# Optimization experiments

Measured on AMD Instinct MI355X. Metric: run time of the kernel, lower is better.

## Reference

```python
import jax, jax.numpy as jnp
import numpy as np

B, S, V, E, H, NL, DFF = 16, 16, 64, 64, 8, 4, 2048
L = S * V
DH = E // H
NUM_GRIDS = 100
POI_DIM = 8
OV_DIM = 8


def setup_inputs() -> dict:
    key = jax.random.key(0)
    ks = jax.random.split(key, 32)
    sc = 0.05
    inp = {}
    inp['features'] = jax.random.normal(ks[0], (B, S, V, 3), jnp.float32)
    inp['overlap_tag'] = jax.random.randint(ks[1], (B, S, V), 0, 3)
    inp['poi_id'] = jax.random.randint(ks[2], (B, S, V), 0, NUM_GRIDS + 1)
    # embedders
    inp['W_raw'] = jax.random.normal(ks[3], (3, E), jnp.float32) * sc
    inp['b_raw'] = jnp.zeros((E,), jnp.float32)
    inp['pos_tab'] = jax.random.normal(ks[4], (S, E), jnp.float32) * sc
    inp['type_tab'] = jax.random.normal(ks[5], (V, E), jnp.float32) * sc
    inp['poi_tab'] = jax.random.normal(ks[6], (NUM_GRIDS + 1, POI_DIM), jnp.float32) * sc
    inp['overlap_tab'] = jax.random.normal(ks[7], (3, OV_DIM), jnp.float32) * sc
    inp['W_comb'] = jax.random.normal(ks[8], (E + OV_DIM + POI_DIM, E), jnp.float32) * sc
    inp['b_comb'] = jnp.zeros((E,), jnp.float32)
    # transformer layers (stacked over NL)
    inp['Wqkv'] = jax.random.normal(ks[9], (NL, E, 3 * E), jnp.float32) * sc
    inp['bqkv'] = jnp.zeros((NL, 3 * E), jnp.float32)
    inp['Wo'] = jax.random.normal(ks[10], (NL, E, E), jnp.float32) * sc
    inp['bo'] = jnp.zeros((NL, E), jnp.float32)
    inp['ln1_s'] = jnp.ones((NL, E), jnp.float32)
    inp['ln1_b'] = jnp.zeros((NL, E), jnp.float32)
    inp['W1'] = jax.random.normal(ks[11], (NL, E, DFF), jnp.float32) * sc
    inp['b1'] = jnp.zeros((NL, DFF), jnp.float32)
    inp['W2'] = jax.random.normal(ks[12], (NL, DFF, E), jnp.float32) * sc
    inp['b2'] = jnp.zeros((NL, E), jnp.float32)
    inp['ln2_s'] = jnp.ones((NL, E), jnp.float32)
    inp['ln2_b'] = jnp.zeros((NL, E), jnp.float32)
    inp['W_head'] = jax.random.normal(ks[13], (E, 3), jnp.float32) * sc
    inp['b_head'] = jnp.zeros((3,), jnp.float32)
    return inp


def _layer_norm(x, s, b):
    m = x.mean(-1, keepdims=True)
    v = ((x - m) ** 2).mean(-1, keepdims=True)
    return (x - m) / jnp.sqrt(v + 1e-5) * s + b


def _forward(features, overlap_tag, poi_id, W_raw, b_raw, pos_tab, type_tab,
             poi_tab, overlap_tab, W_comb, b_comb, Wqkv, bqkv, Wo, bo,
             ln1_s, ln1_b, W1, b1, W2, b2, ln2_s, ln2_b, W_head, b_head):
    # padding_idx=0 rows are zero (as in nn.Embedding(padding_idx=0))
    poi_tab = poi_tab.at[0].set(0.0)
    overlap_tab = overlap_tab.at[0].set(0.0)

    zero_mask = (features.sum(-1) == 0).reshape(B, L)  # [B, L]
    ov_idx = jnp.maximum(overlap_tag, 0)
    poi_idx = jnp.maximum(poi_id, 0)

    feat_e = features @ W_raw + b_raw                    # [B,S,V,E]
    concat = jnp.concatenate([feat_e, overlap_tab[ov_idx], poi_tab[poi_idx]], axis=-1)
    x = (concat @ W_comb + b_comb).reshape(B, L, E)      # [B,L,E]

    t_idx = jnp.repeat(jnp.arange(S), V)                 # [L]
    v_idx = jnp.tile(jnp.arange(V), S)                   # [L]
    struct_mask = (t_idx[:, None] != t_idx[None, :]) & (v_idx[:, None] != v_idx[None, :])
    full_mask = struct_mask[None] | zero_mask[:, None, :] | zero_mask[:, :, None]  # [B,L,L]
    bias = jnp.where(full_mask, -jnp.inf, 0.0)[:, None, :, :]  # [B,1,L,L]

    x = x + pos_tab[t_idx][None] + type_tab[v_idx][None]

    scale = 1.0 / jnp.sqrt(jnp.asarray(DH, x.dtype))
    for l in range(NL):
        qkv = x @ Wqkv[l] + bqkv[l]                      # [B,L,3E]
        q, k, v = jnp.split(qkv, 3, axis=-1)
        q = q.reshape(B, L, H, DH)
        k = k.reshape(B, L, H, DH)
        v = v.reshape(B, L, H, DH)
        scores = jnp.einsum('bqhd,bkhd->bhqk', q, k) * scale + bias
        attn = jax.nn.softmax(scores, axis=-1)
        o = jnp.einsum('bhqk,bkhd->bqhd', attn, v).reshape(B, L, E)
        x = _layer_norm(x + o @ Wo[l] + bo[l], ln1_s[l], ln1_b[l])
        ff = jax.nn.relu(x @ W1[l] + b1[l]) @ W2[l] + b2[l]
        x = _layer_norm(x + ff, ln2_s[l], ln2_b[l])

    last = x.reshape(B, S, V, E)[:, -1]                  # [B,V,E]
    return last @ W_head + b_head                        # [B,V,3]


def reference(features, overlap_tag, poi_id, W_raw, b_raw, pos_tab, type_tab,
              poi_tab, overlap_tab, W_comb, b_comb, Wqkv, bqkv, Wo, bo,
              ln1_s, ln1_b, W1, b1, W2, b2, ln2_s, ln2_b, W_head, b_head):
    return _forward(features, overlap_tag, poi_id, W_raw, b_raw, pos_tab, type_tab,
                    poi_tab, overlap_tab, W_comb, b_comb, Wqkv, bqkv, Wo, bo,
                    ln1_s, ln1_b, W1, b1, W2, b2, ln2_s, ln2_b, W_head, b_head)
```

## Files before the change

kernel.cpp:

```cpp
#include <hip/hip_runtime.h>
#include <math.h>

#define BB 16
#define SS 16
#define VVV 64
#define EE 64
#define HHH 8
#define NLAYER 4
#define DFF_ 2048
#define LL 1024
#define BL 16384
#define PERL 131072

typedef __attribute__((ext_vector_type(8))) _Float16 half8;
typedef __attribute__((ext_vector_type(4))) _Float16 half4v;
typedef __attribute__((ext_vector_type(2))) _Float16 half2v;
typedef __attribute__((ext_vector_type(4))) float f32x4;

#if defined(__has_builtin)
#if __has_builtin(__builtin_amdgcn_fdot2)
#define HAVE_FDOT2 1
#endif
#endif

#define SW64(m, k)  (((m) << 6) + ((((k) >> 3) ^ ((m) & 7)) << 3) + ((k) & 7))


__global__ __launch_bounds__(256) void k_prep(
    const float* __restrict__ W1, const float* __restrict__ W2,
    const float* __restrict__ Wqkv, const float* __restrict__ Wo,
    const float* __restrict__ Wcomb,
    _Float16* __restrict__ w1f, _Float16* __restrict__ w2f,
    _Float16* __restrict__ wqkvf, _Float16* __restrict__ wof,
    _Float16* __restrict__ wcombt)
{
  __shared__ float t[64 * 65];
  int bx = blockIdx.x;
  int cc = threadIdx.x & 63, rr = threadIdx.x >> 6;

  if (bx >= 272) {
    int r0 = (bx - 272) * 64;
#pragma unroll
    for (int i = 0; i < 16; i++) {
      int r = i * 4 + rr;
      if (r0 + r < 80) t[r * 65 + cc] = Wcomb[(size_t)(r0 + r) * 64 + cc];
    }
    __syncthreads();
#pragma unroll
    for (int i = 0; i < 16; i++) {
      int c = i * 4 + rr;
      if (r0 + c < 80) wcombt[(size_t)cc * 80 + r0 + c] = (_Float16)t[c * 65 + cc];
    }
    return;
  }

  const float* src; _Float16* dst; int astr;
  if (bx < 128) {
    int l = bx >> 5, g = bx & 31;
    src = W1 + (size_t)l * PERL + g * 64; astr = 2048;
    dst = w1f + (size_t)(l * 32 + g) * 4096;
  } else if (bx < 256) {
    int j = bx - 128; int l = j >> 5, g = j & 31;
    src = W2 + (size_t)l * PERL + (size_t)g * 64 * 64; astr = 64;
    dst = w2f + (size_t)(l * 32 + g) * 4096;
  } else if (bx < 268) {
    int j = bx - 256; int l = j / 3, g = j % 3;
    src = Wqkv + (size_t)l * 64 * 192 + g * 64; astr = 192;
    dst = wqkvf + (size_t)(l * 3 + g) * 4096;
  } else {
    int l = bx - 268;
    src = Wo + (size_t)l * 4096; astr = 64;
    dst = wof + (size_t)l * 4096;
  }
#pragma unroll
  for (int i = 0; i < 16; i++) {
    int a = i * 4 + rr;
    t[cc * 65 + a] = src[(size_t)a * astr + cc];
  }
  __syncthreads();
#pragma unroll
  for (int it = 0; it < 2; it++) {
    int c = threadIdx.x + it * 256;
    int frag = c >> 6, lane = c & 63;
    int m = (frag >> 1) * 16 + (lane & 15);
    int k0 = (frag & 1) * 32 + (lane >> 4) * 8;
    const float* tr = &t[m * 65 + k0];
    half8 h;
#pragma unroll
    for (int j = 0; j < 8; j++) h[j] = (_Float16)tr[j];
    *(half8*)&dst[(size_t)c * 8] = h;
  }
}

__device__ __forceinline__ void qkv_nb(
    const half8 (&af)[2][2], const _Float16* __restrict__ wqkvf,
    const float* __restrict__ bqkv, _Float16* __restrict__ qbuf,
    _Float16* __restrict__ kbuf, _Float16* __restrict__ vbuf,
    int bx, int nb, int wm, int wn, int lane)
{
  int quad = lane >> 4, l15 = lane & 15;
  const _Float16* bt = wqkvf + (size_t)nb * 4096;
  half8 bf[2][2];
#pragma unroll
  for (int nt = 0; nt < 2; nt++)
#pragma unroll
    for (int ks = 0; ks < 2; ks++)
      bf[nt][ks] = *(const half8*)&bt[(size_t)(((wn * 2 + nt) * 2 + ks) * 512) +
                                      lane * 8];
  f32x4 acc[2][2];
#pragma unroll
  for (int mt = 0; mt < 2; mt++)
#pragma unroll
    for (int nt = 0; nt < 2; nt++) {
      float bv = bqkv[nb * 64 + wn * 32 + nt * 16 + l15];
      acc[mt][nt] = (f32x4){bv, bv, bv, bv};
    }
#pragma unroll
  for (int ks = 0; ks < 2; ks++)
#pragma unroll
    for (int mt = 0; mt < 2; mt++)
#pragma unroll
      for (int nt = 0; nt < 2; nt++)
        acc[mt][nt] = __builtin_amdgcn_mfma_f32_16x16x32_f16(
            af[mt][ks], bf[nt][ks], acc[mt][nt], 0, 0, 0);
  _Float16* dst = (nb == 0) ? qbuf : ((nb == 1) ? kbuf : vbuf);
#pragma unroll
  for (int mt = 0; mt < 2; mt++)
#pragma unroll
    for (int nt = 0; nt < 2; nt++) {
      int col = wn * 32 + nt * 16 + l15;
      int h = col >> 3, d = col & 7;
#pragma unroll
      for (int r = 0; r < 4; r++) {
        int row = bx * 64 + wm * 32 + mt * 16 + quad * 4 + r;
        int b = row >> 10, rb = row & 1023;
        dst[((size_t)(b * 8 + h) * 1024 + rb) * 8 + d] = (_Float16)acc[mt][nt][r];
      }
    }
}

__device__ __forceinline__ void ffn_load2(
    const _Float16* __restrict__ w1f, const _Float16* __restrict__ w2f, int g,
    half8 (&a1)[2][2], half8 (&b2w)[2][2], int wn, int lane)
{
  const _Float16* w1t_ = w1f + (size_t)g * 4096;
  const _Float16* w2t_ = w2f + (size_t)g * 4096;
#pragma unroll
  for (int ht = 0; ht < 2; ht++)
#pragma unroll
    for (int ks = 0; ks < 2; ks++)
      a1[ht][ks] = *(const half8*)&w1t_[(size_t)(((wn * 2 + ht) * 2 + ks) * 512) +
                                        lane * 8];
#pragma unroll
  for (int nt = 0; nt < 2; nt++)
#pragma unroll
    for (int ks = 0; ks < 2; ks++)
      b2w[nt][ks] = *(const half8*)&w2t_[(size_t)(((wn * 2 + nt) * 2 + ks) * 512) +
                                         lane * 8];
}

__device__ __forceinline__ void ffn_step2(
    const half8 (&a1)[2][2], const half8 (&b2w)[2][2], const half8 (&xb)[2][2],
    _Float16* hsbuf, const float* __restrict__ b1, int g, f32x4 (&acc)[2][2],
    int wn, int lane)
{
  int quad = lane >> 4, l15 = lane & 15;
  f32x4 hacc[2][2];
#pragma unroll
  for (int ht = 0; ht < 2; ht++)
#pragma unroll
    for (int mt = 0; mt < 2; mt++) hacc[ht][mt] = (f32x4){0.f, 0.f, 0.f, 0.f};
#pragma unroll
  for (int ks = 0; ks < 2; ks++)
#pragma unroll
    for (int ht = 0; ht < 2; ht++)
#pragma unroll
      for (int mt = 0; mt < 2; mt++)
        hacc[ht][mt] = __builtin_amdgcn_mfma_f32_16x16x32_f16(
            a1[ht][ks], xb[mt][ks], hacc[ht][mt], 0, 0, 0);
#pragma unroll
  for (int ht = 0; ht < 2; ht++) {
    float4 bb = *(const float4*)&b1[g * 64 + wn * 32 + ht * 16 + quad * 4];
#pragma unroll
    for (int mt = 0; mt < 2; mt++) {
      f32x4 hv = hacc[ht][mt];
      half4v hp = (half4v){
          (_Float16)fmaxf(hv[0] + bb.x, 0.f), (_Float16)fmaxf(hv[1] + bb.y, 0.f),
          (_Float16)fmaxf(hv[2] + bb.z, 0.f), (_Float16)fmaxf(hv[3] + bb.w, 0.f)};
      *(half4v*)&hsbuf[SW64(mt * 16 + l15, wn * 32 + ht * 16 + quad * 4)] = hp;
    }
  }
  __syncthreads();
#pragma unroll
  for (int ks = 0; ks < 2; ks++)
#pragma unroll
    for (int mt = 0; mt < 2; mt++) {
      half8 a2 = *(const half8*)&hsbuf[SW64(mt * 16 + l15, ks * 32 + quad * 8)];
#pragma unroll
      for (int nt = 0; nt < 2; nt++)
        acc[mt][nt] = __builtin_amdgcn_mfma_f32_16x16x32_f16(a2, b2w[nt][ks],
                                                             acc[mt][nt], 0, 0, 0);
    }
}

__global__ __launch_bounds__(256) void k_embqkv(
    const float* __restrict__ features, const int* __restrict__ ovtag,
    const int* __restrict__ poiid, const float* __restrict__ W_raw,
    const float* __restrict__ b_raw, const float* __restrict__ ov_tab,
    const float* __restrict__ poi_tab, const _Float16* __restrict__ wcombt,
    const float* __restrict__ b_comb, const float* __restrict__ pos_tab,
    const float* __restrict__ type_tab, float* __restrict__ x1,
    float* __restrict__ zm, const _Float16* __restrict__ wqkvf,
    const float* __restrict__ bqkv, _Float16* __restrict__ qbuf,
    _Float16* __restrict__ kbuf, _Float16* __restrict__ vbuf)
{
  constexpr int KP = 104;
  __shared__ _Float16 As[64 * KP];
  __shared__ _Float16 Bs[64 * KP];
  __shared__ _Float16 xs[4096];
  int tid = threadIdx.x;
  int bx = blockIdx.x;
  int m0 = bx * 64;
  int wave = tid >> 6, lane = tid & 63, quad = lane >> 4, l15 = lane & 15;
  int wm = wave >> 1, wn = wave & 1;
  for (int p = tid; p < 1536; p += 256) {
    int r = p / 24, s = p - r * 24; int c = s * 4;
    int row = m0 + r;
    float f0 = features[row * 3 + 0];
    float f1 = features[row * 3 + 1];
    float f2 = features[row * 3 + 2];
    if (s == 0) zm[row] = ((f0 + f1 + f2) == 0.f) ? 1.f : 0.f;
    half4v h;
#pragma unroll
    for (int j = 0; j < 4; j++) {
      int cc = c + j; float v;
      if (cc < 64) {
        v = b_raw[cc] + f0 * W_raw[cc] + f1 * W_raw[64 + cc] + f2 * W_raw[128 + cc];
      } else if (cc < 72) {
        int tt = ovtag[row]; v = (tt <= 0) ? 0.f : ov_tab[tt * 8 + cc - 64];
      } else if (cc < 80) {
        int tt = poiid[row]; v = (tt <= 0) ? 0.f : poi_tab[tt * 8 + cc - 72];
      } else v = 0.f;
      h[j] = (_Float16)v;
    }
    *(half4v*)&As[r * KP + c] = h;
  }
  for (int p = tid; p < 1536; p += 256) {
    int r = p / 24, s = p - r * 24; int c = s * 4;
    half4v h = (half4v){0, 0, 0, 0};
    if (c < 80) h = *(const half4v*)&wcombt[r * 80 + c];
    *(half4v*)&Bs[r * KP + c] = h;
  }
  __syncthreads();
  f32x4 acc[2][2];
#pragma unroll
  for (int mt = 0; mt < 2; mt++)
#pragma unroll
    for (int nt = 0; nt < 2; nt++) {
      float bv = b_comb[wn * 32 + nt * 16 + l15];
      acc[mt][nt] = (f32x4){bv, bv, bv, bv};
    }
#pragma unroll
  for (int ks = 0; ks < 3; ks++) {
    half8 af[2], bf[2];
#pragma unroll
    for (int mt = 0; mt < 2; mt++)
      af[mt] = *(const half8*)&As[(wm * 32 + mt * 16 + l15) * KP + ks * 32 + quad * 8];
#pragma unroll
    for (int nt = 0; nt < 2; nt++)
      bf[nt] = *(const half8*)&Bs[(wn * 32 + nt * 16 + l15) * KP + ks * 32 + quad * 8];
#pragma unroll
    for (int mt = 0; mt < 2; mt++)
#pragma unroll
      for (int nt = 0; nt < 2; nt++)
        acc[mt][nt] = __builtin_amdgcn_mfma_f32_16x16x32_f16(af[mt], bf[nt],
                                                             acc[mt][nt], 0, 0, 0);
  }
#pragma unroll
  for (int mt = 0; mt < 2; mt++)
#pragma unroll
    for (int nt = 0; nt < 2; nt++)
#pragma unroll
      for (int r = 0; r < 4; r++) {
        int lrow = wm * 32 + mt * 16 + quad * 4 + r;
        int row = m0 + lrow;
        int col = wn * 32 + nt * 16 + l15;
        int l = row & (LL - 1);
        float v = acc[mt][nt][r] +
            pos_tab[(l >> 6) * 64 + col] + type_tab[(l & 63) * 64 + col];
        x1[(size_t)row * 64 + col] = v;
        xs[SW64(lrow, col)] = (_Float16)v;
      }
  __syncthreads();
  half8 af[2][2];
#pragma unroll
  for (int mt = 0; mt < 2; mt++)
#pragma unroll
    for (int ks = 0; ks < 2; ks++)
      af[mt][ks] = *(const half8*)&xs[SW64(wm * 32 + mt * 16 + l15,
                                           ks * 32 + quad * 8)];
  for (int nb = 0; nb < 3; nb++)
    qkv_nb(af, wqkvf, bqkv, qbuf, kbuf, vbuf, bx, nb, wm, wn, lane);
}

__global__ __launch_bounds__(128) void k_attn3(
    const _Float16* __restrict__ qbuf, const _Float16* __restrict__ kbuf,
    const _Float16* __restrict__ vbuf, const float* __restrict__ zm,
    _Float16* __restrict__ obuf)
{
  __shared__ _Float16 Ks[1024 * 8];
  __shared__ _Float16 Vs[1024 * 8];
  __shared__ float zs[1024];
  int blk = blockIdx.x;
  int qb = blk & 7, h = (blk >> 3) & 7, b = blk >> 6;
  int qrow = qb * 128 + threadIdx.x;
  half8 qh = *(const half8*)&qbuf[(size_t)(b * 8 + h) * 8192 + (size_t)qrow * 8];
  const _Float16* kb = kbuf + (size_t)(b * 8 + h) * 8192;
  const _Float16* vb = vbuf + (size_t)(b * 8 + h) * 8192;
  for (int p = threadIdx.x; p < 1024; p += 128) {
    *(half8*)&Ks[p * 8] = *(const half8*)&kb[p * 8];
    *(half8*)&Vs[p * 8] = *(const half8*)&vb[p * 8];
    zs[p] = zm[b * LL + p];
  }
  __syncthreads();
  int tq = qrow >> 6, vq = qrow & 63;
  const float scale = 0.3535533905932738f;
  float m = -INFINITY, lsum = 0.f;
  float acc[8] = {0.f, 0.f, 0.f, 0.f, 0.f, 0.f, 0.f, 0.f};
  bool zmq = (zs[qrow] != 0.f);

  auto attend = [&](int k) {
    if (zs[k] != 0.f) return;
    half8 kk = *(const half8*)&Ks[k * 8];
    float s = 0.f;
#ifdef HAVE_FDOT2
#pragma unroll
    for (int j = 0; j < 4; j++) {
      half2v qa = (half2v){qh[2 * j], qh[2 * j + 1]};
      half2v ka = (half2v){kk[2 * j], kk[2 * j + 1]};
      s = __builtin_amdgcn_fdot2(qa, ka, s, false);
    }
#else
#pragma unroll
    for (int j = 0; j < 8; j++) s += (float)qh[j] * (float)kk[j];
#endif
    s *= scale;
    half8 vv = *(const half8*)&Vs[k * 8];
    float nm = fmaxf(m, s);
    float r = __expf(m - nm);
    float p = __expf(s - nm);
    lsum = lsum * r + p;
#pragma unroll
    for (int d = 0; d < 8; d++) acc[d] = acc[d] * r + p * (float)vv[d];
    m = nm;
  };

  if (!zmq) {
    for (int vv = 0; vv < 64; vv++) attend(tq * 64 + vv);
    for (int tt = 0; tt < 16; tt++) {
      if (tt == tq) continue;
      attend(tt * 64 + vq);
    }
  }
  float inv = 1.f / lsum;
  half8 o;
#pragma unroll
  for (int d = 0; d < 8; d++) o[d] = (_Float16)(acc[d] * inv);
  size_t tile = (size_t)(b * 16 + (qrow >> 6));
  int frag = ((qrow >> 4) & 3) * 2 + (h >> 2);
  int flane = (h & 3) * 16 + (qrow & 15);
  *(half8*)&obuf[tile * 4096 + frag * 512 + flane * 8] = o;
}

__global__ __launch_bounds__(256, 2) void k_layer2(
    const _Float16* __restrict__ obuf, const _Float16* __restrict__ wof,
    const float* __restrict__ bo, float* __restrict__ x1,
    const float* __restrict__ ln1_s, const float* __restrict__ ln1_b,
    const _Float16* __restrict__ w1f, const _Float16* __restrict__ w2f,
    const float* __restrict__ b1, const float* __restrict__ b2,
    const float* __restrict__ ln2_s, const float* __restrict__ ln2_b,
    const _Float16* __restrict__ wqkvf, const float* __restrict__ bqkv,
    _Float16* __restrict__ qbuf, _Float16* __restrict__ kbuf,
    _Float16* __restrict__ vbuf, int doqkv,
    const float* __restrict__ Wh, const float* __restrict__ bh,
    float* __restrict__ out)
{
  __shared__ float ots[32 * 68];
  __shared__ _Float16 xs[2048];
  __shared__ float x2f[2048];
  __shared__ _Float16 hs[2][2][2048];
  int tid = threadIdx.x;
  int bx = blockIdx.x;
  int r0 = bx * 32;
  int wave = tid >> 6, lane = tid & 63;
  int quad = lane >> 4, l15 = lane & 15;
  int grp = wave >> 1, wn = wave & 1;

  {
    const _Float16* ot = obuf + (size_t)(bx >> 1) * 4096;
    int mt_g = (bx & 1) * 2 + grp;
    half8 af[2], bf[2][2];
#pragma unroll
    for (int ks = 0; ks < 2; ks++)
      af[ks] = *(const half8*)&ot[(size_t)((mt_g * 2 + ks) * 512) + lane * 8];
#pragma unroll
    for (int nt = 0; nt < 2; nt++)
#pragma unroll
      for (int ks = 0; ks < 2; ks++)
        bf[nt][ks] = *(const half8*)&wof[(size_t)(((wn * 2 + nt) * 2 + ks) * 512) +
                                         lane * 8];
    f32x4 acc[2];
#pragma unroll
    for (int nt = 0; nt < 2; nt++) {
      float bv = bo[wn * 32 + nt * 16 + l15];
      acc[nt] = (f32x4){bv, bv, bv, bv};
    }
#pragma unroll
    for (int ks = 0; ks < 2; ks++)
#pragma unroll
      for (int nt = 0; nt < 2; nt++)
        acc[nt] = __builtin_amdgcn_mfma_f32_16x16x32_f16(af[ks], bf[nt][ks],
                                                         acc[nt], 0, 0, 0);
#pragma unroll
    for (int nt = 0; nt < 2; nt++)
#pragma unroll
      for (int r = 0; r < 4; r++)
        ots[(grp * 16 + quad * 4 + r) * 68 + wn * 32 + nt * 16 + l15] = acc[nt][r];
  }
  __syncthreads();
  for (int i = 0; i < 8; i++) {
    int row = wave * 8 + i;
    size_t off = (size_t)(r0 + row) * 64 + lane;
    float val = ots[row * 68 + lane] + x1[off];
    float sum = val;
#pragma unroll
    for (int o = 32; o > 0; o >>= 1) sum += __shfl_xor(sum, o);
    float mean = sum * (1.f / 64.f);
    float d = val - mean;
    float sq = d * d;
#pragma unroll
    for (int o = 32; o > 0; o >>= 1) sq += __shfl_xor(sq, o);
    float xv = d * rsqrtf(sq * (1.f / 64.f) + 1e-5f) * ln1_s[lane] + ln1_b[lane];
    x2f[row * 64 + lane] = xv;
    xs[SW64(row, lane)] = (_Float16)xv;
  }
  __syncthreads();

  half8 xb[2][2];
#pragma unroll
  for (int mt = 0; mt < 2; mt++)
#pragma unroll
    for (int ks = 0; ks < 2; ks++)
      xb[mt][ks] = *(const half8*)&xs[SW64(mt * 16 + l15, ks * 32 + quad * 8)];
  f32x4 acc[2][2];
#pragma unroll
  for (int mt = 0; mt < 2; mt++)
#pragma unroll
    for (int nt = 0; nt < 2; nt++) {
      float bv = (grp == 0) ? b2[wn * 32 + nt * 16 + l15] : 0.f;
      acc[mt][nt] = (f32x4){bv, bv, bv, bv};
    }
  half8 a1x[2][2], b2x[2][2], a1y[2][2], b2y[2][2];
  ffn_load2(w1f, w2f, grp, a1x, b2x, wn, lane);
  for (int ii = 0; ii < 8; ii++) {
    ffn_load2(w1f, w2f, ii * 4 + 2 + grp, a1y, b2y, wn, lane);
    ffn_step2(a1x, b2x, xb, &hs[grp][0][0], b1, ii * 4 + grp, acc, wn, lane);
    if (ii < 7) ffn_load2(w1f, w2f, ii * 4 + 4 + grp, a1x, b2x, wn, lane);
    ffn_step2(a1y, b2y, xb, &hs[grp][1][0], b1, ii * 4 + 2 + grp, acc, wn, lane);
  }
  __syncthreads();
  if (grp == 0) {
#pragma unroll
    for (int mt = 0; mt < 2; mt++)
#pragma unroll
      for (int nt = 0; nt < 2; nt++)
#pragma unroll
        for (int r = 0; r < 4; r++)
          ots[(mt * 16 + quad * 4 + r) * 68 + wn * 32 + nt * 16 + l15] =
              acc[mt][nt][r];
  }
  __syncthreads();
  if (grp == 1) {
#pragma unroll
    for (int mt = 0; mt < 2; mt++)
#pragma unroll
      for (int nt = 0; nt < 2; nt++)
#pragma unroll
        for (int r = 0; r < 4; r++)
          ots[(mt * 16 + quad * 4 + r) * 68 + wn * 32 + nt * 16 + l15] +=
              acc[mt][nt][r];
  }
  __syncthreads();
  for (int i = 0; i < 8; i++) {
    int row = wave * 8 + i;
    size_t off = (size_t)(r0 + row) * 64 + lane;
    float val = ots[row * 68 + lane] + x2f[row * 64 + lane];
    float sum = val;
#pragma unroll
    for (int o = 32; o > 0; o >>= 1) sum += __shfl_xor(sum, o);
    float mean = sum * (1.f / 64.f);
    float d = val - mean;
    float sq = d * d;
#pragma unroll
    for (int o = 32; o > 0; o >>= 1) sq += __shfl_xor(sq, o);
    float xv = d * rsqrtf(sq * (1.f / 64.f) + 1e-5f) * ln2_s[lane] + ln2_b[lane];
    x1[off] = xv;
    x2f[row * 64 + lane] = xv;
    xs[SW64(row, lane)] = (_Float16)xv;
  }
  if (!doqkv) {
    __syncthreads();
    if ((bx & 31) >= 30 && tid < 96) {
      int b = bx >> 5;
      int i = tid / 3, j = tid - i * 3;
      int vglob = (bx & 1) * 32 + i;
      float a = bh[j];
      for (int e = 0; e < 64; e++)
        a += x2f[i * 64 + e] * Wh[e * 3 + j];
      out[((size_t)(b * 64 + vglob)) * 3 + j] = a;
    }
    return;
  }
  __syncthreads();
  half8 af[2][2];
#pragma unroll
  for (int mt = 0; mt < 2; mt++)
#pragma unroll
    for (int ks = 0; ks < 2; ks++)
      af[mt][ks] = *(const half8*)&xs[SW64(mt * 16 + l15, ks * 32 + quad * 8)];
  for (int nb = 0; nb < 3; nb++) {
    const _Float16* bt = wqkvf + (size_t)nb * 4096;
    half8 bf[2];
#pragma unroll
    for (int ks = 0; ks < 2; ks++)
      bf[ks] = *(const half8*)&bt[(size_t)((wave * 2 + ks) * 512) + lane * 8];
    f32x4 qacc[2];
#pragma unroll
    for (int mt = 0; mt < 2; mt++) {
      float bv = bqkv[nb * 64 + wave * 16 + l15];
      qacc[mt] = (f32x4){bv, bv, bv, bv};
    }
#pragma unroll
    for (int ks = 0; ks < 2; ks++)
#pragma unroll
      for (int mt = 0; mt < 2; mt++)
        qacc[mt] = __builtin_amdgcn_mfma_f32_16x16x32_f16(af[mt][ks], bf[ks],
                                                          qacc[mt], 0, 0, 0);
    _Float16* dst = (nb == 0) ? qbuf : ((nb == 1) ? kbuf : vbuf);
    int col = wave * 16 + l15;
    int h = col >> 3, d = col & 7;
#pragma unroll
    for (int mt = 0; mt < 2; mt++)
#pragma unroll
      for (int r = 0; r < 4; r++) {
        int row = r0 + mt * 16 + quad * 4 + r;
        int b = row >> 10, rb = row & 1023;
        dst[((size_t)(b * 8 + h) * 1024 + rb) * 8 + d] = (_Float16)qacc[mt][r];
      }
  }
}

extern "C" void kernel_launch(void* const* d_in, const int* in_sizes, int n_in,
                              void* d_out, int out_size, void* d_ws, size_t ws_size,
                              hipStream_t stream) {
  const float* features = (const float*)d_in[0];
  const int*   ovtag    = (const int*)d_in[1];
  const int*   poiid    = (const int*)d_in[2];
  const float* W_raw    = (const float*)d_in[3];
  const float* b_raw    = (const float*)d_in[4];
  const float* pos_tab  = (const float*)d_in[5];
  const float* type_tab = (const float*)d_in[6];
  const float* poi_tab  = (const float*)d_in[7];
  const float* ov_tab   = (const float*)d_in[8];
  const float* W_comb   = (const float*)d_in[9];
  const float* b_comb   = (const float*)d_in[10];
  const float* Wqkv     = (const float*)d_in[11];
  const float* bqkv     = (const float*)d_in[12];
  const float* Wo       = (const float*)d_in[13];
  const float* bo       = (const float*)d_in[14];
  const float* ln1_s    = (const float*)d_in[15];
  const float* ln1_b    = (const float*)d_in[16];
  const float* W1       = (const float*)d_in[17];
  const float* b1       = (const float*)d_in[18];
  const float* W2       = (const float*)d_in[19];
  const float* b2       = (const float*)d_in[20];
  const float* ln2_s    = (const float*)d_in[21];
  const float* ln2_b    = (const float*)d_in[22];
  const float* W_head   = (const float*)d_in[23];
  const float* b_head   = (const float*)d_in[24];
  float* out = (float*)d_out;
  float* ws  = (float*)d_ws;

  float* zm  = ws;
  float* x1  = zm + BL;
  _Float16* qbuf   = (_Float16*)(x1 + (size_t)BL * 64);
  _Float16* kbuf   = qbuf + (size_t)BL * 64;
  _Float16* vbuf   = kbuf + (size_t)BL * 64;
  _Float16* obuf16 = vbuf + (size_t)BL * 64;
  _Float16* wcombt = obuf16 + (size_t)BL * 64;
  _Float16* w1f    = wcombt + 5120;
  _Float16* w2f    = w1f + (size_t)NLAYER * PERL;
  _Float16* wqkvf  = w2f + (size_t)NLAYER * PERL;
  _Float16* wof    = wqkvf + (size_t)NLAYER * 3 * 4096;

  k_prep<<<274, 256, 0, stream>>>(W1, W2, Wqkv, Wo, W_comb,
                                  w1f, w2f, wqkvf, wof, wcombt);
  k_embqkv<<<256, 256, 0, stream>>>(features, ovtag, poiid, W_raw, b_raw,
                                    ov_tab, poi_tab, wcombt, b_comb,
                                    pos_tab, type_tab, x1, zm,
                                    wqkvf, bqkv, qbuf, kbuf, vbuf);
  for (int l = 0; l < NLAYER; l++) {
    k_attn3<<<1024, 128, 0, stream>>>(qbuf, kbuf, vbuf, zm, obuf16);
    int doqkv = (l < NLAYER - 1);
    k_layer2<<<512, 256, 0, stream>>>(
        obuf16, wof + (size_t)l * 4096, bo + l * EE, x1,
        ln1_s + l * EE, ln1_b + l * EE,
        w1f + (size_t)l * PERL, w2f + (size_t)l * PERL,
        b1 + l * DFF_, b2 + l * EE,
        ln2_s + l * EE, ln2_b + l * EE,
        wqkvf + (size_t)(l + 1 < NLAYER ? l + 1 : 0) * 3 * 4096,
        bqkv + (l + 1 < NLAYER ? l + 1 : 0) * 192,
        qbuf, kbuf, vbuf, doqkv, W_head, b_head, out);
  }
}
```

Baseline: 305.3 us.

## Fuse attention into the per-layer MLP kernel with ping-pong QKV buffers

Removes the separate attention kernel and computes each block's 32 query rows across all 8 heads inside the layer kernel. K and V are now read straight from global memory instead of being staged in shared memory. The attention output stays in shared memory and feeds the Wo MFMA directly, so the obuf round trip and one launch per layer go away. QKV buffers alternate between two sets to avoid a read/write race across blocks. The cost is uncached global gathers for K/V and an extra shared allocation in a kernel limited to two blocks per unit.

```diff
diff --git a/kernel.cpp b/kernel.cpp
--- a/kernel.cpp
+++ b/kernel.cpp
@@ -303,106 +303,96 @@
     qkv_nb(af, wqkvf, bqkv, qbuf, kbuf, vbuf, bx, nb, wm, wn, lane);
 }
 
-__global__ __launch_bounds__(128) void k_attn3(
-    const _Float16* __restrict__ qbuf, const _Float16* __restrict__ kbuf,
-    const _Float16* __restrict__ vbuf, const float* __restrict__ zm,
-    _Float16* __restrict__ obuf)
-{
-  __shared__ _Float16 Ks[1024 * 8];
-  __shared__ _Float16 Vs[1024 * 8];
-  __shared__ float zs[1024];
-  int blk = blockIdx.x;
-  int qb = blk & 7, h = (blk >> 3) & 7, b = blk >> 6;
-  int qrow = qb * 128 + threadIdx.x;
-  half8 qh = *(const half8*)&qbuf[(size_t)(b * 8 + h) * 8192 + (size_t)qrow * 8];
-  const _Float16* kb = kbuf + (size_t)(b * 8 + h) * 8192;
-  const _Float16* vb = vbuf + (size_t)(b * 8 + h) * 8192;
-  for (int p = threadIdx.x; p < 1024; p += 128) {
-    *(half8*)&Ks[p * 8] = *(const half8*)&kb[p * 8];
-    *(half8*)&Vs[p * 8] = *(const half8*)&vb[p * 8];
-    zs[p] = zm[b * LL + p];
-  }
-  __syncthreads();
-  int tq = qrow >> 6, vq = qrow & 63;
-  const float scale = 0.3535533905932738f;
-  float m = -INFINITY, lsum = 0.f;
-  float acc[8] = {0.f, 0.f, 0.f, 0.f, 0.f, 0.f, 0.f, 0.f};
-  bool zmq = (zs[qrow] != 0.f);
-
-  auto attend = [&](int k) {
-    if (zs[k] != 0.f) return;
-    half8 kk = *(const half8*)&Ks[k * 8];
-    float s = 0.f;
-#ifdef HAVE_FDOT2
-#pragma unroll
-    for (int j = 0; j < 4; j++) {
-      half2v qa = (half2v){qh[2 * j], qh[2 * j + 1]};
-      half2v ka = (half2v){kk[2 * j], kk[2 * j + 1]};
-      s = __builtin_amdgcn_fdot2(qa, ka, s, false);
-    }
-#else
-#pragma unroll
-    for (int j = 0; j < 8; j++) s += (float)qh[j] * (float)kk[j];
-#endif
-    s *= scale;
-    half8 vv = *(const half8*)&Vs[k * 8];
-    float nm = fmaxf(m, s);
-    float r = __expf(m - nm);
-    float p = __expf(s - nm);
-    lsum = lsum * r + p;
-#pragma unroll
-    for (int d = 0; d < 8; d++) acc[d] = acc[d] * r + p * (float)vv[d];
-    m = nm;
-  };
-
-  if (!zmq) {
-    for (int vv = 0; vv < 64; vv++) attend(tq * 64 + vv);
-    for (int tt = 0; tt < 16; tt++) {
-      if (tt == tq) continue;
-      attend(tt * 64 + vq);
-    }
-  }
-  float inv = 1.f / lsum;
-  half8 o;
-#pragma unroll
-  for (int d = 0; d < 8; d++) o[d] = (_Float16)(acc[d] * inv);
-  size_t tile = (size_t)(b * 16 + (qrow >> 6));
-  int frag = ((qrow >> 4) & 3) * 2 + (h >> 2);
-  int flane = (h & 3) * 16 + (qrow & 15);
-  *(half8*)&obuf[tile * 4096 + frag * 512 + flane * 8] = o;
-}
-
-__global__ __launch_bounds__(256, 2) void k_layer2(
-    const _Float16* __restrict__ obuf, const _Float16* __restrict__ wof,
-    const float* __restrict__ bo, float* __restrict__ x1,
+__global__ __launch_bounds__(256, 2) void k_layerf(
+    const _Float16* __restrict__ qin, const _Float16* __restrict__ kin,
+    const _Float16* __restrict__ vin, const float* __restrict__ zm,
+    const _Float16* __restrict__ wof, const float* __restrict__ bo,
+    float* __restrict__ x1,
     const float* __restrict__ ln1_s, const float* __restrict__ ln1_b,
     const _Float16* __restrict__ w1f, const _Float16* __restrict__ w2f,
     const float* __restrict__ b1, const float* __restrict__ b2,
     const float* __restrict__ ln2_s, const float* __restrict__ ln2_b,
     const _Float16* __restrict__ wqkvf, const float* __restrict__ bqkv,
-    _Float16* __restrict__ qbuf, _Float16* __restrict__ kbuf,
-    _Float16* __restrict__ vbuf, int doqkv,
+    _Float16* __restrict__ qout, _Float16* __restrict__ kout,
+    _Float16* __restrict__ vout, int doqkv,
     const float* __restrict__ Wh, const float* __restrict__ bh,
     float* __restrict__ out)
 {
   __shared__ float ots[32 * 68];
-  __shared__ _Float16 xs[2048];
+  __shared__ __align__(16) _Float16 xs[2048];
   __shared__ float x2f[2048];
-  __shared__ _Float16 hs[2][2][2048];
+  __shared__ __align__(16) _Float16 hs[2][2][2048];
+  __shared__ __align__(16) _Float16 os[2048];
+  __shared__ float zsh[1024];
   int tid = threadIdx.x;
   int bx = blockIdx.x;
   int r0 = bx * 32;
   int wave = tid >> 6, lane = tid & 63;
   int quad = lane >> 4, l15 = lane & 15;
   int grp = wave >> 1, wn = wave & 1;
+  int b = r0 >> 10;
+
+  for (int p = tid; p < 1024; p += 256) zsh[p] = zm[b * LL + p];
+  __syncthreads();
 
   {
-    const _Float16* ot = obuf + (size_t)(bx >> 1) * 4096;
-    int mt_g = (bx & 1) * 2 + grp;
+    int lr = tid & 31, hh = tid >> 5;
+    int rb = (r0 & 1023) + lr;
+    int tq = rb >> 6, vq = rb & 63;
+    const _Float16* kb = kin + (size_t)(b * 8 + hh) * 8192;
+    const _Float16* vb = vin + (size_t)(b * 8 + hh) * 8192;
+    half8 qh = *(const half8*)&qin[(size_t)(b * 8 + hh) * 8192 + (size_t)rb * 8];
+    const float scale = 0.3535533905932738f;
+    float m = -INFINITY, lsum = 0.f;
+    float acc[8] = {0.f, 0.f, 0.f, 0.f, 0.f, 0.f, 0.f, 0.f};
+    bool zmq = (zsh[rb] != 0.f);
+
+    auto attend = [&](int k) {
+      if (zsh[k] != 0.f) return;
+      half8 kk = *(const half8*)&kb[(size_t)k * 8];
+      float s = 0.f;
+#ifdef HAVE_FDOT2
+#pragma unroll
+      for (int j = 0; j < 4; j++) {
+        half2v qa = (half2v){qh[2 * j], qh[2 * j + 1]};
+        half2v ka = (half2v){kk[2 * j], kk[2 * j + 1]};
+        s = __builtin_amdgcn_fdot2(qa, ka, s, false);
+      }
+#else
+#pragma unroll
+      for (int j = 0; j < 8; j++) s += (float)qh[j] * (float)kk[j];
+#endif
+      s *= scale;
+      half8 vv = *(const half8*)&vb[(size_t)k * 8];
+      float nm = fmaxf(m, s);
+      float r = __expf(m - nm);
+      float p = __expf(s - nm);
+      lsum = lsum * r + p;
+#pragma unroll
+      for (int d = 0; d < 8; d++) acc[d] = acc[d] * r + p * (float)vv[d];
+      m = nm;
+    };
+
+    if (!zmq) {
+      for (int vv2 = 0; vv2 < 64; vv2++) attend(tq * 64 + vv2);
+      for (int tt = 0; tt < 16; tt++) {
+        if (tt == tq) continue;
+        attend(tt * 64 + vq);
+      }
+    }
+    float inv = 1.f / lsum;
+    half8 o;
+#pragma unroll
+    for (int d = 0; d < 8; d++) o[d] = (_Float16)(acc[d] * inv);
+    *(half8*)&os[SW64(lr, hh * 8)] = o;
+  }
+  __syncthreads();
+
+  {
     half8 af[2], bf[2][2];
 #pragma unroll
     for (int ks = 0; ks < 2; ks++)
-      af[ks] = *(const half8*)&ot[(size_t)((mt_g * 2 + ks) * 512) + lane * 8];
+      af[ks] = *(const half8*)&os[SW64(grp * 16 + l15, ks * 32 + quad * 8)];
 #pragma unroll
     for (int nt = 0; nt < 2; nt++)
 #pragma unroll
@@ -511,13 +501,13 @@
   if (!doqkv) {
     __syncthreads();
     if ((bx & 31) >= 30 && tid < 96) {
-      int b = bx >> 5;
+      int bb2 = bx >> 5;
       int i = tid / 3, j = tid - i * 3;
       int vglob = (bx & 1) * 32 + i;
       float a = bh[j];
       for (int e = 0; e < 64; e++)
         a += x2f[i * 64 + e] * Wh[e * 3 + j];
-      out[((size_t)(b * 64 + vglob)) * 3 + j] = a;
+      out[((size_t)(bb2 * 64 + vglob)) * 3 + j] = a;
     }
     return;
   }
@@ -546,16 +536,16 @@
       for (int mt = 0; mt < 2; mt++)
         qacc[mt] = __builtin_amdgcn_mfma_f32_16x16x32_f16(af[mt][ks], bf[ks],
                                                           qacc[mt], 0, 0, 0);
-    _Float16* dst = (nb == 0) ? qbuf : ((nb == 1) ? kbuf : vbuf);
+    _Float16* dst = (nb == 0) ? qout : ((nb == 1) ? kout : vout);
     int col = wave * 16 + l15;
-    int h = col >> 3, d = col & 7;
+    int h2 = col >> 3, d2 = col & 7;
 #pragma unroll
     for (int mt = 0; mt < 2; mt++)
 #pragma unroll
       for (int r = 0; r < 4; r++) {
         int row = r0 + mt * 16 + quad * 4 + r;
-        int b = row >> 10, rb = row & 1023;
-        dst[((size_t)(b * 8 + h) * 1024 + rb) * 8 + d] = (_Float16)qacc[mt][r];
+        int rbq = row & 1023;
+        dst[((size_t)(b * 8 + h2) * 1024 + rbq) * 8 + d2] = (_Float16)qacc[mt][r];
       }
   }
 }
@@ -593,11 +583,13 @@
 
   float* zm  = ws;
   float* x1  = zm + BL;
-  _Float16* qbuf   = (_Float16*)(x1 + (size_t)BL * 64);
-  _Float16* kbuf   = qbuf + (size_t)BL * 64;
-  _Float16* vbuf   = kbuf + (size_t)BL * 64;
-  _Float16* obuf16 = vbuf + (size_t)BL * 64;
-  _Float16* wcombt = obuf16 + (size_t)BL * 64;
+  _Float16* qbA = (_Float16*)(x1 + (size_t)BL * 64);
+  _Float16* kbA = qbA + (size_t)BL * 64;
+  _Float16* vbA = kbA + (size_t)BL * 64;
+  _Float16* qbB = vbA + (size_t)BL * 64;
+  _Float16* kbB = qbB + (size_t)BL * 64;
+  _Float16* vbB = kbB + (size_t)BL * 64;
+  _Float16* wcombt = vbB + (size_t)BL * 64;
   _Float16* w1f    = wcombt + 5120;
   _Float16* w2f    = w1f + (size_t)NLAYER * PERL;
   _Float16* wqkvf  = w2f + (size_t)NLAYER * PERL;
@@ -608,18 +600,24 @@
   k_embqkv<<<256, 256, 0, stream>>>(features, ovtag, poiid, W_raw, b_raw,
                                     ov_tab, poi_tab, wcombt, b_comb,
                                     pos_tab, type_tab, x1, zm,
-                                    wqkvf, bqkv, qbuf, kbuf, vbuf);
+                                    wqkvf, bqkv, qbA, kbA, vbA);
   for (int l = 0; l < NLAYER; l++) {
-    k_attn3<<<1024, 128, 0, stream>>>(qbuf, kbuf, vbuf, zm, obuf16);
+    const _Float16* qin = (l & 1) ? qbB : qbA;
+    const _Float16* kin = (l & 1) ? kbB : kbA;
+    const _Float16* vin = (l & 1) ? vbB : vbA;
+    _Float16* qout = (l & 1) ? qbA : qbB;
+    _Float16* kout = (l & 1) ? kbA : kbB;
+    _Float16* vout = (l & 1) ? vbA : vbB;
     int doqkv = (l < NLAYER - 1);
-    k_layer2<<<512, 256, 0, stream>>>(
-        obuf16, wof + (size_t)l * 4096, bo + l * EE, x1,
+    k_layerf<<<512, 256, 0, stream>>>(
+        qin, kin, vin, zm,
+        wof + (size_t)l * 4096, bo + l * EE, x1,
         ln1_s + l * EE, ln1_b + l * EE,
         w1f + (size_t)l * PERL, w2f + (size_t)l * PERL,
         b1 + l * DFF_, b2 + l * EE,
         ln2_s + l * EE, ln2_b + l * EE,
         wqkvf + (size_t)(l + 1 < NLAYER ? l + 1 : 0) * 3 * 4096,
         bqkv + (l + 1 < NLAYER ? l + 1 : 0) * 192,
-        qbuf, kbuf, vbuf, doqkv, W_head, b_head, out);
+        qout, kout, vout, doqkv, W_head, b_head, out);
   }
 }
```

After: 310.1 us. Within noise of the previous version (+1.6%).
